# Performance work log

Hardware: AMD Instinct MI355X
Metric: run time of the kernel (lower is better)

The kernel has to match this reference:

```python
import jax, jax.numpy as jnp
import numpy as np

B, ENC, DEC, TSTEPS, PRED = 512, 2048, 1024, 12, 24
IN_DIM = ENC + 1 + TSTEPS  # 2061


def setup_inputs() -> dict:
    key = jax.random.key(0)
    ks = jax.random.split(key, 12)
    s = 0.05  # small init scale for numerical stability
    return {
        "encoder_out": jax.random.normal(ks[0], (B, ENC), jnp.float32),
        "oni_input": jax.random.normal(ks[1], (B, 1), jnp.float32),
        "ssi": jax.random.normal(ks[2], (B, TSTEPS), jnp.float32),
        "W_ih": jax.random.normal(ks[3], (4 * DEC, IN_DIM), jnp.float32) * s,
        "b_ih": jax.random.normal(ks[4], (4 * DEC,), jnp.float32) * s,
        "W_hh": jax.random.normal(ks[5], (4 * DEC, DEC), jnp.float32) * s,
        "b_hh": jax.random.normal(ks[6], (4 * DEC,), jnp.float32) * s,
        "W_l1": jax.random.normal(ks[7], (DEC, DEC * PRED), jnp.float32) * s,
        "b_l1": jax.random.normal(ks[8], (DEC,), jnp.float32) * s,
        "W_l2": jax.random.normal(ks[9], (DEC, DEC), jnp.float32) * s,
        "b_l2": jax.random.normal(ks[10], (DEC,), jnp.float32) * s,
    }


def reference(encoder_out, oni_input, ssi, W_ih, b_ih, W_hh, b_hh, W_l1, b_l1, W_l2, b_l2):
    # cfg.lstm=True, cfg.loss_criterion='enso', dropout p=0 (identity)
    x = jnp.concatenate([encoder_out, oni_input, ssi], axis=1)  # (B, IN_DIM)
    # input is identical every step: precompute input projection once
    x_proj = x @ W_ih.T + b_ih + b_hh  # (B, 4*DEC)
    D = W_hh.shape[1]
    T = W_l1.shape[1] // D
    b = x.shape[0]

    def step(carry, _):
        h, c = carry
        gates = x_proj + h @ W_hh.T  # (B, 4D), PyTorch gate order i,f,g,o
        i, f, g, o = jnp.split(gates, 4, axis=1)
        c = jax.nn.sigmoid(f) * c + jax.nn.sigmoid(i) * jnp.tanh(g)
        h = jax.nn.sigmoid(o) * jnp.tanh(c)
        return (h, c), h

    init = (jnp.zeros((b, D), x.dtype), jnp.zeros((b, D), x.dtype))
    _, hs = jax.lax.scan(step, init, None, length=T)  # (T, B, D)
    # torch.stack(dim=2) then flatten(start_dim=1) -> layout (B, D*T)
    preds = jnp.transpose(hs, (1, 2, 0)).reshape(b, D * T)
    preds = jax.nn.sigmoid(preds @ W_l1.T + b_l1)
    preds = preds @ W_l2.T + b_l2
    return jax.nn.sigmoid(preds)  # 'enso' head; dropout(p=0) is identity
```

## Files before the change

kernel.cpp:

```cpp
#include <hip/hip_runtime.h>
#include <hip/hip_bf16.h>

#define BSZ   512
#define ENCD  2048
#define DECD  1024
#define TST   12
#define PREDT 24
#define INDIM 2061
#define KPAD  2112
#define G4    4096
#define KH    24576

typedef __attribute__((ext_vector_type(8))) short s8v;
typedef __attribute__((ext_vector_type(4))) short s4v;
typedef __attribute__((ext_vector_type(4))) float f4v;

__device__ __forceinline__ short bf16_of(float f) {
  union { float f; unsigned u; } x; x.f = f;
  unsigned r = x.u + 0x7fffu + ((x.u >> 16) & 1u);
  return (short)(r >> 16);
}
__device__ __forceinline__ float sigf(float x) { return 1.f / (1.f + __expf(-x)); }
__device__ __forceinline__ float tanh_(float x) { return 1.f - 2.f / (1.f + __expf(2.f * x)); }

__device__ __forceinline__ int lds_off(int row, int colb) {
  return row * 128 + (colb ^ ((row & 7) << 4));
}


__global__ void prep_x(const float* __restrict__ enc, const float* __restrict__ oni,
                       const float* __restrict__ ssi, short* __restrict__ x_bf) {
  int idx = blockIdx.x * 256 + threadIdx.x;
  if (idx >= BSZ * KPAD) return;
  int b = idx / KPAD, k = idx % KPAD;
  float v = 0.f;
  if (k < ENCD) v = enc[b * ENCD + k];
  else if (k == ENCD) v = oni[b];
  else if (k < INDIM) v = ssi[b * TST + (k - ENCD - 1)];
  x_bf[idx] = bf16_of(v);
}

__global__ void prep_wih(const float* __restrict__ W, short* __restrict__ o) {
  int idx = blockIdx.x * 256 + threadIdx.x;
  int rp = idx / KPAD; int k = idx - rp * KPAD;
  int dblk = rp >> 6, rem = rp & 63, g = rem >> 4, dl = rem & 15;
  int srow = g * 1024 + dblk * 16 + dl;
  float v = (k < INDIM) ? W[(size_t)srow * INDIM + k] : 0.f;
  o[idx] = bf16_of(v);
}

__global__ void prep_whh(const float* __restrict__ W, short* __restrict__ o) {
  int idx = blockIdx.x * 256 + threadIdx.x;
  int rp = idx >> 10; int k = idx & 1023;
  int dblk = rp >> 6, rem = rp & 63, g = rem >> 4, dl = rem & 15;
  int srow = g * 1024 + dblk * 16 + dl;
  o[idx] = bf16_of(W[(size_t)srow * 1024 + k]);
}

__global__ __launch_bounds__(256, 1) void xproj_k(
    const short* __restrict__ x_bf, const short* __restrict__ wih_bf,
    const float* __restrict__ b_ih, const float* __restrict__ b_hh,
    float* __restrict__ xp_p) {
  __shared__ __align__(16) char sA[2][16384];
  __shared__ __align__(16) char sB[2][8192];
  int tid = threadIdx.x, lane = tid & 63, w = tid >> 6;
  int L = blockIdx.x;
  int bm = L >> 6, pb = (L & 7) * 8 + ((L >> 3) & 7);
  const int l4 = lane & 15, lg = lane >> 4;

  s8v aR[4], bR[2];
  auto LOAD = [&](int kt) {
    int kk = kt * 64;
#pragma unroll
    for (int i = 0; i < 4; ++i) {
      int c = tid + i * 256, r = c >> 3, sl = c & 7;
      aR[i] = *(const s8v*)(x_bf + (size_t)(bm * 128 + r) * KPAD + kk + sl * 8);
    }
#pragma unroll
    for (int i = 0; i < 2; ++i) {
      int c = tid + i * 256, r = c >> 3, sl = c & 7;
      bR[i] = *(const s8v*)(wih_bf + (size_t)(pb * 64 + r) * KPAD + kk + sl * 8);
    }
  };
  auto WRITE = [&](int buf) {
#pragma unroll
    for (int i = 0; i < 4; ++i) {
      int c = tid + i * 256, r = c >> 3, sl = c & 7;
      *(s8v*)(sA[buf] + lds_off(r, sl * 16)) = aR[i];
    }
#pragma unroll
    for (int i = 0; i < 2; ++i) {
      int c = tid + i * 256, r = c >> 3, sl = c & 7;
      *(s8v*)(sB[buf] + lds_off(r, sl * 16)) = bR[i];
    }
  };

  f4v acc[2][4] = {};
  LOAD(0); WRITE(0); LOAD(1);
  __syncthreads();
  for (int kt = 0; kt < 33; ++kt) {
    int cur = kt & 1;
    if (kt < 32) WRITE(cur ^ 1);
    if (kt < 31) LOAD(kt + 2);
#pragma unroll
    for (int ks = 0; ks < 2; ++ks) {
      int colb = ks * 64 + lg * 16;
      s8v af[2], bf[4];
#pragma unroll
      for (int mi = 0; mi < 2; ++mi)
        af[mi] = *(const s8v*)(sA[cur] + lds_off(w * 32 + mi * 16 + l4, colb));
#pragma unroll
      for (int ni = 0; ni < 4; ++ni)
        bf[ni] = *(const s8v*)(sB[cur] + lds_off(ni * 16 + l4, colb));
#pragma unroll
      for (int mi = 0; mi < 2; ++mi)
#pragma unroll
        for (int ni = 0; ni < 4; ++ni)
          acc[mi][ni] = __builtin_amdgcn_mfma_f32_16x16x32_bf16(af[mi], bf[ni], acc[mi][ni], 0, 0, 0);
    }
    __syncthreads();
  }
#pragma unroll
  for (int ni = 0; ni < 4; ++ni) {
    int src = ni * 1024 + pb * 16 + l4;
    float bv = b_ih[src] + b_hh[src];
#pragma unroll
    for (int mi = 0; mi < 2; ++mi)
#pragma unroll
      for (int j = 0; j < 4; ++j) {
        int row = bm * 128 + w * 32 + mi * 16 + lg * 4 + j;
        xp_p[(size_t)row * G4 + pb * 64 + ni * 16 + l4] = acc[mi][ni][j] + bv;
      }
  }
}

template <bool FIRST>
__global__ __launch_bounds__(256, 2) void step_k(
    const short* __restrict__ h_in, const short* __restrict__ whh_bf,
    const float* __restrict__ xp_p, float* __restrict__ c_st,
    short* __restrict__ h_out, short* __restrict__ hs_t, int tstep) {
  __shared__ __align__(16) char sB[2][8192];
  __shared__ __align__(16) char sA[4][2][2048];
  int tid = threadIdx.x, lane = tid & 63, w = tid >> 6;
  int L = blockIdx.x;
  int bm = L >> 6, dblk = (L & 7) * 8 + ((L >> 3) & 7);
  const int l4 = lane & 15, lg = lane >> 4;

  f4v acc[4] = {};

  if (!FIRST) {
    const short* hbase = h_in + (size_t)(bm * 64 + w * 16) * DECD;
    const short* bbase = whh_bf + (size_t)(dblk * 64) * DECD;
    s8v aR[2], bR[2];
    auto LOAD = [&](int kt) {
      int kk = kt * 64;
#pragma unroll
      for (int i = 0; i < 2; ++i) {
        int c = lane + i * 64, r = c >> 3, sl = c & 7;
        aR[i] = *(const s8v*)(hbase + (size_t)r * DECD + kk + sl * 8);
      }
#pragma unroll
      for (int i = 0; i < 2; ++i) {
        int c = tid + i * 256, r = c >> 3, sl = c & 7;
        bR[i] = *(const s8v*)(bbase + (size_t)r * DECD + kk + sl * 8);
      }
    };
    auto WRITE = [&](int buf) {
#pragma unroll
      for (int i = 0; i < 2; ++i) {
        int c = lane + i * 64, r = c >> 3, sl = c & 7;
        *(s8v*)(sA[w][buf] + lds_off(r, sl * 16)) = aR[i];
      }
#pragma unroll
      for (int i = 0; i < 2; ++i) {
        int c = tid + i * 256, r = c >> 3, sl = c & 7;
        *(s8v*)(sB[buf] + lds_off(r, sl * 16)) = bR[i];
      }
    };
    LOAD(0); WRITE(0); LOAD(1);
    __syncthreads();
    for (int kt = 0; kt < 16; ++kt) {
      int cur = kt & 1;
      if (kt < 15) WRITE(cur ^ 1);
      if (kt < 14) LOAD(kt + 2);
#pragma unroll
      for (int ks = 0; ks < 2; ++ks) {
        int colb = ks * 64 + lg * 16;
        s8v af = *(const s8v*)(sA[w][cur] + lds_off(l4, colb));
        s8v bf[4];
#pragma unroll
        for (int ni = 0; ni < 4; ++ni)
          bf[ni] = *(const s8v*)(sB[cur] + lds_off(ni * 16 + l4, colb));
#pragma unroll
        for (int ni = 0; ni < 4; ++ni)
          acc[ni] = __builtin_amdgcn_mfma_f32_16x16x32_bf16(af, bf[ni], acc[ni], 0, 0, 0);
      }
      __syncthreads();
    }
  }

  int d = dblk * 16 + l4;
#pragma unroll
  for (int j = 0; j < 4; ++j) {
    int row = bm * 64 + w * 16 + lg * 4 + j;
    size_t xb = (size_t)row * G4 + dblk * 64 + l4;
    float gi = acc[0][j] + xp_p[xb];
    float gf = acc[1][j] + xp_p[xb + 16];
    float gg = acc[2][j] + xp_p[xb + 32];
    float go = acc[3][j] + xp_p[xb + 48];
    size_t cd = (size_t)row * DECD + d;
    float c_old = FIRST ? 0.f : c_st[cd];
    float cn = sigf(gf) * c_old + sigf(gi) * tanh_(gg);
    c_st[cd] = cn;
    float h = sigf(go) * tanh_(cn);
    short hb = bf16_of(h);
    if (tstep < 23) h_out[cd] = hb;
    hs_t[(size_t)tstep * (BSZ * DECD) + cd] = hb;
  }
}

__global__ void transpose_k(const short* __restrict__ hs_t, short* __restrict__ hs) {
  int g = blockIdx.x * 256 + threadIdx.x;
  int row = g >> 10, d = g & 1023;
#pragma unroll
  for (int i = 0; i < 3; ++i) {
    s8v v;
#pragma unroll
    for (int u = 0; u < 8; ++u)
      v[u] = hs_t[(size_t)(i * 8 + u) * (BSZ * DECD) + (size_t)row * DECD + d];
    *(s8v*)(hs + (size_t)row * KH + d * PREDT + i * 8) = v;
  }
}

template <int EPI>
__global__ __launch_bounds__(256, 2) void gemm2_k(
    const short* __restrict__ A, int lda, const float* __restrict__ Bw, int ldb,
    int ntiles, int kchunk, const float* __restrict__ bias1,
    float* __restrict__ Cf, int ldc) {
  __shared__ __align__(16) char sA[2][16384];
  __shared__ __align__(16) char sB[2][16384];
  int tid = threadIdx.x, lane = tid & 63, wid = tid >> 6;
  int wr = wid >> 1, wc = wid & 1, l4 = lane & 15, lg = lane >> 4;
  int bm = blockIdx.x * 128, bn = blockIdx.y * 128;
  int k0 = blockIdx.z * kchunk;
  size_t zoff = (size_t)blockIdx.z * BSZ * (size_t)ldc;
  s8v aR[4]; f4v bR[4][2];
  auto LOAD = [&](int kt) {
    int kk = k0 + kt * 64;
#pragma unroll
    for (int i = 0; i < 4; ++i) {
      int c = tid + i * 256, r = c >> 3, sl = c & 7;
      aR[i] = *(const s8v*)(A + (size_t)(bm + r) * lda + kk + sl * 8);
      const float* src = Bw + (size_t)(bn + r) * ldb + kk + sl * 8;
      bR[i][0] = *(const f4v*)src;
      bR[i][1] = *(const f4v*)(src + 4);
    }
  };
  auto WRITE = [&](int buf) {
#pragma unroll
    for (int i = 0; i < 4; ++i) {
      int c = tid + i * 256, r = c >> 3, sl = c & 7;
      *(s8v*)(sA[buf] + lds_off(r, sl * 16)) = aR[i];
      s8v v;
#pragma unroll
      for (int j = 0; j < 4; ++j) { v[j] = bf16_of(bR[i][0][j]); v[4 + j] = bf16_of(bR[i][1][j]); }
      *(s8v*)(sB[buf] + lds_off(r, sl * 16)) = v;
    }
  };
  f4v acc[4][4] = {};
  LOAD(0); WRITE(0);
  if (ntiles > 1) LOAD(1);
  __syncthreads();
  for (int kt = 0; kt < ntiles; ++kt) {
    int cur = kt & 1;
    if (kt + 1 < ntiles) WRITE(cur ^ 1);
    if (kt + 2 < ntiles) LOAD(kt + 2);
#pragma unroll
    for (int ks = 0; ks < 2; ++ks) {
      int colb = ks * 64 + lg * 16;
      s8v af[4], bf[4];
#pragma unroll
      for (int mi = 0; mi < 4; ++mi)
        af[mi] = *(const s8v*)(sA[cur] + lds_off(wr * 64 + mi * 16 + l4, colb));
#pragma unroll
      for (int ni = 0; ni < 4; ++ni)
        bf[ni] = *(const s8v*)(sB[cur] + lds_off(wc * 64 + ni * 16 + l4, colb));
#pragma unroll
      for (int mi = 0; mi < 4; ++mi)
#pragma unroll
        for (int ni = 0; ni < 4; ++ni)
          acc[mi][ni] = __builtin_amdgcn_mfma_f32_16x16x32_bf16(af[mi], bf[ni], acc[mi][ni], 0, 0, 0);
    }
    __syncthreads();
  }
#pragma unroll
  for (int mi = 0; mi < 4; ++mi)
#pragma unroll
    for (int ni = 0; ni < 4; ++ni)
#pragma unroll
      for (int j = 0; j < 4; ++j) {
        int row = bm + wr * 64 + mi * 16 + lg * 4 + j;
        int col = bn + wc * 64 + ni * 16 + l4;
        float v = acc[mi][ni][j];
        if (EPI == 1) Cf[zoff + (size_t)row * ldc + col] = v;
        else Cf[(size_t)row * ldc + col] = sigf(v + bias1[col]);
      }
}

__global__ void reduce16(const float* __restrict__ part, const float* __restrict__ b_l1,
                         short* __restrict__ z1) {
  int i4 = blockIdx.x * 256 + threadIdx.x;
  int base = i4 * 4;
  int n = base & (DECD - 1);
  f4v s = *(const f4v*)(b_l1 + n);
#pragma unroll
  for (int z = 0; z < 16; ++z) {
    f4v p = *(const f4v*)(part + (size_t)z * (BSZ * DECD) + base);
#pragma unroll
    for (int j = 0; j < 4; ++j) s[j] += p[j];
  }
  s4v o;
#pragma unroll
  for (int j = 0; j < 4; ++j) o[j] = bf16_of(sigf(s[j]));
  *(s4v*)(z1 + base) = o;
}


extern "C" void kernel_launch(void* const* d_in, const int* in_sizes, int n_in,
                              void* d_out, int out_size, void* d_ws, size_t ws_size,
                              hipStream_t stream) {
  const float* enc  = (const float*)d_in[0];
  const float* oni  = (const float*)d_in[1];
  const float* ssi  = (const float*)d_in[2];
  const float* W_ih = (const float*)d_in[3];
  const float* b_ih = (const float*)d_in[4];
  const float* W_hh = (const float*)d_in[5];
  const float* b_hh = (const float*)d_in[6];
  const float* W_l1 = (const float*)d_in[7];
  const float* b_l1 = (const float*)d_in[8];
  const float* W_l2 = (const float*)d_in[9];
  const float* b_l2 = (const float*)d_in[10];
  float* out = (float*)d_out;
  (void)in_sizes; (void)n_in; (void)out_size; (void)ws_size;

  char* ws = (char*)d_ws;
  size_t off = 0;
  auto carve = [&](size_t bytes) { char* p = ws + off; off += (bytes + 255) & ~(size_t)255; return p; };
  short* x_bf   = (short*)carve((size_t)BSZ * KPAD * 2);
  short* wih_bf = (short*)carve((size_t)G4 * KPAD * 2);
  short* whh_bf = (short*)carve((size_t)G4 * DECD * 2);
  float* xp_p   = (float*)carve((size_t)BSZ * G4 * 4);
  short* h0     = (short*)carve((size_t)BSZ * DECD * 2);
  short* h1     = (short*)carve((size_t)BSZ * DECD * 2);
  float* c_st   = (float*)carve((size_t)BSZ * DECD * 4);
  float* part   = (float*)ws;
  if (off < (size_t)16 * BSZ * DECD * 4) off = (((size_t)16 * BSZ * DECD * 4) + 255) & ~(size_t)255;
  short* hs_t   = (short*)carve((size_t)PREDT * BSZ * DECD * 2);
  short* hs     = (short*)carve((size_t)BSZ * KH * 2);
  short* z1     = (short*)carve((size_t)BSZ * DECD * 2);

  prep_x  <<<(BSZ * KPAD) / 256, 256, 0, stream>>>(enc, oni, ssi, x_bf);
  prep_wih<<<(G4 * KPAD) / 256, 256, 0, stream>>>(W_ih, wih_bf);
  prep_whh<<<(G4 * DECD) / 256, 256, 0, stream>>>(W_hh, whh_bf);

  xproj_k<<<256, 256, 0, stream>>>(x_bf, wih_bf, b_ih, b_hh, xp_p);

  step_k<true><<<512, 256, 0, stream>>>(nullptr, whh_bf, xp_p, c_st, h0, hs_t, 0);
  for (int t = 1; t < PREDT; ++t) {
    short* hr = (t & 1) ? h0 : h1;
    short* hw = (t & 1) ? h1 : h0;
    step_k<false><<<512, 256, 0, stream>>>(hr, whh_bf, xp_p, c_st, hw, hs_t, t);
  }

  transpose_k<<<(BSZ * DECD) / 256, 256, 0, stream>>>(hs_t, hs);

  gemm2_k<1><<<dim3(4, 8, 16), 256, 0, stream>>>(hs, KH, W_l1, KH, 24, KH / 16, nullptr, part, DECD);
  reduce16<<<(BSZ * DECD) / 1024, 256, 0, stream>>>(part, b_l1, z1);

  gemm2_k<2><<<dim3(4, 8, 1), 256, 0, stream>>>(z1, DECD, W_l2, DECD, 16, DECD, b_l2, out, DECD);
}
```

Measured before the change: 412.0 us.

## Restructure LSTM step kernel with split-K warps and direct A loads; reorder GEMM grid

The recurrent step kernel now gives each block a 64-row batch tile and a 64-gate column tile. Its four waves split K in two halves, and each wave computes a 32x64 tile, so every W_hh tile staged in LDS feeds twice as many MFMAs. The h operand is read directly from global memory instead of being staged through LDS. Partial sums are reduced through shared memory, and the gate epilogue is remapped so lanes read swizzled LDS rows, which coalesces xp/c/h accesses. The output GEMMs swap grid x/y so blocks sharing a weight tile launch adjacently, aiming for better L2 reuse; unstaged global A loads may add latency.

```diff
diff --git a/kernel.cpp b/kernel.cpp
--- a/kernel.cpp
+++ b/kernel.cpp
@@ -139,75 +139,107 @@
     const short* __restrict__ h_in, const short* __restrict__ whh_bf,
     const float* __restrict__ xp_p, float* __restrict__ c_st,
     short* __restrict__ h_out, short* __restrict__ hs_t, int tstep) {
-  __shared__ __align__(16) char sB[2][8192];
-  __shared__ __align__(16) char sA[4][2][2048];
+  __shared__ __align__(16) char sB[32768];
+  __shared__ __align__(16) char sX[16384];
   int tid = threadIdx.x, lane = tid & 63, w = tid >> 6;
-  int L = blockIdx.x;
-  int bm = L >> 6, dblk = (L & 7) * 8 + ((L >> 3) & 7);
+  int kg = w >> 1, ow = w & 1;
+  int bm = blockIdx.x, cp = blockIdx.y;
   const int l4 = lane & 15, lg = lane >> 4;
 
-  f4v acc[4] = {};
+  f4v acc[2][4] = {};
 
   if (!FIRST) {
-    const short* hbase = h_in + (size_t)(bm * 64 + w * 16) * DECD;
-    const short* bbase = whh_bf + (size_t)(dblk * 64) * DECD;
-    s8v aR[2], bR[2];
-    auto LOAD = [&](int kt) {
-      int kk = kt * 64;
-#pragma unroll
-      for (int i = 0; i < 2; ++i) {
-        int c = lane + i * 64, r = c >> 3, sl = c & 7;
-        aR[i] = *(const s8v*)(hbase + (size_t)r * DECD + kk + sl * 8);
-      }
-#pragma unroll
-      for (int i = 0; i < 2; ++i) {
-        int c = tid + i * 256, r = c >> 3, sl = c & 7;
-        bR[i] = *(const s8v*)(bbase + (size_t)r * DECD + kk + sl * 8);
+    const short* bbase = whh_bf + (size_t)cp * 64 * DECD + kg * 512;
+    const short* abase = h_in + (size_t)(bm * 64 + ow * 32) * DECD + kg * 512;
+    char* myB = sB + kg * 16384;
+    int lc = tid & 127;
+    s8v st[4];
+    auto LOADB = [&](int kt) {
+#pragma unroll
+      for (int i = 0; i < 4; ++i) {
+        int c = lc + i * 128, r = c >> 3, sl = c & 7;
+        st[i] = *(const s8v*)(bbase + (size_t)r * DECD + kt * 64 + sl * 8);
       }
     };
-    auto WRITE = [&](int buf) {
-#pragma unroll
-      for (int i = 0; i < 2; ++i) {
-        int c = lane + i * 64, r = c >> 3, sl = c & 7;
-        *(s8v*)(sA[w][buf] + lds_off(r, sl * 16)) = aR[i];
-      }
-#pragma unroll
-      for (int i = 0; i < 2; ++i) {
-        int c = tid + i * 256, r = c >> 3, sl = c & 7;
-        *(s8v*)(sB[buf] + lds_off(r, sl * 16)) = bR[i];
+    auto WRITEB = [&](int buf) {
+      char* p = myB + buf * 8192;
+#pragma unroll
+      for (int i = 0; i < 4; ++i) {
+        int c = lc + i * 128, r = c >> 3, sl = c & 7;
+        *(s8v*)(p + lds_off(r, sl * 16)) = st[i];
       }
     };
-    LOAD(0); WRITE(0); LOAD(1);
+    LOADB(0); WRITEB(0); LOADB(1);
     __syncthreads();
-    for (int kt = 0; kt < 16; ++kt) {
+    for (int kt = 0; kt < 8; ++kt) {
       int cur = kt & 1;
-      if (kt < 15) WRITE(cur ^ 1);
-      if (kt < 14) LOAD(kt + 2);
+      if (kt < 7) WRITEB(cur ^ 1);
+      if (kt < 6) LOADB(kt + 2);
+      char* p = myB + cur * 8192;
 #pragma unroll
       for (int ks = 0; ks < 2; ++ks) {
-        int colb = ks * 64 + lg * 16;
-        s8v af = *(const s8v*)(sA[w][cur] + lds_off(l4, colb));
-        s8v bf[4];
+        s8v af[2], bf[4];
+#pragma unroll
+        for (int mi = 0; mi < 2; ++mi)
+          af[mi] = *(const s8v*)(abase + (size_t)(mi * 16 + l4) * DECD + kt * 64 + ks * 32 + lg * 8);
 #pragma unroll
         for (int ni = 0; ni < 4; ++ni)
-          bf[ni] = *(const s8v*)(sB[cur] + lds_off(ni * 16 + l4, colb));
-#pragma unroll
-        for (int ni = 0; ni < 4; ++ni)
-          acc[ni] = __builtin_amdgcn_mfma_f32_16x16x32_bf16(af, bf[ni], acc[ni], 0, 0, 0);
+          bf[ni] = *(const s8v*)(p + lds_off(ni * 16 + l4, ks * 64 + lg * 16));
+#pragma unroll
+        for (int mi = 0; mi < 2; ++mi)
+#pragma unroll
+          for (int ni = 0; ni < 4; ++ni)
+            acc[mi][ni] = __builtin_amdgcn_mfma_f32_16x16x32_bf16(af[mi], bf[ni], acc[mi][ni], 0, 0, 0);
       }
       __syncthreads();
     }
-  }
-
-  int d = dblk * 16 + l4;
-#pragma unroll
-  for (int j = 0; j < 4; ++j) {
-    int row = bm * 64 + w * 16 + lg * 4 + j;
-    size_t xb = (size_t)row * G4 + dblk * 64 + l4;
-    float gi = acc[0][j] + xp_p[xb];
-    float gf = acc[1][j] + xp_p[xb + 16];
-    float gg = acc[2][j] + xp_p[xb + 32];
-    float go = acc[3][j] + xp_p[xb + 48];
+    if (kg == 1) {
+#pragma unroll
+      for (int mi = 0; mi < 2; ++mi)
+#pragma unroll
+        for (int ni = 0; ni < 4; ++ni)
+#pragma unroll
+          for (int j = 0; j < 4; ++j)
+            *(float*)(sX + ow * 8192 + ((mi * 4 + ni) * 4 + j) * 256 + lane * 4) = acc[mi][ni][j];
+    }
+    __syncthreads();
+    if (kg == 0) {
+#pragma unroll
+      for (int mi = 0; mi < 2; ++mi)
+#pragma unroll
+        for (int ni = 0; ni < 4; ++ni) {
+#pragma unroll
+          for (int j = 0; j < 4; ++j) {
+            float v = acc[mi][ni][j] +
+                      *(const float*)(sX + ow * 8192 + ((mi * 4 + ni) * 4 + j) * 256 + lane * 4);
+            int row = ow * 32 + mi * 16 + lg * 4 + j;
+            int col = ni * 16 + l4;
+            *(float*)(sB + row * 256 + ((col ^ ((row & 3) << 4)) * 4)) = v;
+          }
+        }
+    }
+    __syncthreads();
+  }
+
+#pragma unroll
+  for (int q = 0; q < 4; ++q) {
+    int idx = tid + q * 256;
+    int r = idx >> 4, dl = idx & 15;
+    int row = bm * 64 + r;
+    size_t xb = (size_t)row * G4 + cp * 64 + dl;
+    float g0 = 0.f, g1 = 0.f, g2 = 0.f, g3 = 0.f;
+    if (!FIRST) {
+      int sw = (r & 3) << 4;
+      g0 = *(const float*)(sB + r * 256 + (((0  + dl) ^ sw) * 4));
+      g1 = *(const float*)(sB + r * 256 + (((16 + dl) ^ sw) * 4));
+      g2 = *(const float*)(sB + r * 256 + (((32 + dl) ^ sw) * 4));
+      g3 = *(const float*)(sB + r * 256 + (((48 + dl) ^ sw) * 4));
+    }
+    float gi = g0 + xp_p[xb];
+    float gf = g1 + xp_p[xb + 16];
+    float gg = g2 + xp_p[xb + 32];
+    float go = g3 + xp_p[xb + 48];
+    int d = cp * 16 + dl;
     size_t cd = (size_t)row * DECD + d;
     float c_old = FIRST ? 0.f : c_st[cd];
     float cn = sigf(gf) * c_old + sigf(gi) * tanh_(gg);
@@ -241,7 +273,7 @@
   __shared__ __align__(16) char sB[2][16384];
   int tid = threadIdx.x, lane = tid & 63, wid = tid >> 6;
   int wr = wid >> 1, wc = wid & 1, l4 = lane & 15, lg = lane >> 4;
-  int bm = blockIdx.x * 128, bn = blockIdx.y * 128;
+  int bn = blockIdx.x * 128, bm = blockIdx.y * 128;
   int k0 = blockIdx.z * kchunk;
   size_t zoff = (size_t)blockIdx.z * BSZ * (size_t)ldc;
   s8v aR[4]; f4v bR[4][2];
@@ -365,17 +397,17 @@
 
   xproj_k<<<256, 256, 0, stream>>>(x_bf, wih_bf, b_ih, b_hh, xp_p);
 
-  step_k<true><<<512, 256, 0, stream>>>(nullptr, whh_bf, xp_p, c_st, h0, hs_t, 0);
+  step_k<true><<<dim3(8, 64), 256, 0, stream>>>(nullptr, whh_bf, xp_p, c_st, h0, hs_t, 0);
   for (int t = 1; t < PREDT; ++t) {
     short* hr = (t & 1) ? h0 : h1;
     short* hw = (t & 1) ? h1 : h0;
-    step_k<false><<<512, 256, 0, stream>>>(hr, whh_bf, xp_p, c_st, hw, hs_t, t);
+    step_k<false><<<dim3(8, 64), 256, 0, stream>>>(hr, whh_bf, xp_p, c_st, hw, hs_t, t);
   }
 
   transpose_k<<<(BSZ * DECD) / 256, 256, 0, stream>>>(hs_t, hs);
 
-  gemm2_k<1><<<dim3(4, 8, 16), 256, 0, stream>>>(hs, KH, W_l1, KH, 24, KH / 16, nullptr, part, DECD);
+  gemm2_k<1><<<dim3(8, 4, 16), 256, 0, stream>>>(hs, KH, W_l1, KH, 24, KH / 16, nullptr, part, DECD);
   reduce16<<<(BSZ * DECD) / 1024, 256, 0, stream>>>(part, b_l1, z1);
 
-  gemm2_k<2><<<dim3(4, 8, 1), 256, 0, stream>>>(z1, DECD, W_l2, DECD, 16, DECD, b_l2, out, DECD);
-}
+  gemm2_k<2><<<dim3(8, 4, 1), 256, 0, stream>>>(z1, DECD, W_l2, DECD, 16, DECD, b_l2, out, DECD);
+}
```

After: 541.7 us. +31.5%, slower.

## Deepen LSTM step K-tile, prefetch gate inputs early, remap grids for weight locality

Applied to the files above, without the earlier changes.

The recurrent step kernel now loads 128-wide K tiles with a 16-row XOR swizzle, which halves the number of pipeline iterations and barriers. It also prefetches the x-projection gate values and the previous cell state into registers before the MFMA loop, so their global latency overlaps the matmul. The step grid becomes 2D (column-block by batch-block), replacing the old interleaved block mapping. In the output GEMMs the grid axes are swapped so that blocks sharing a weight tile are adjacent. LDS usage per block doubles, which may reduce occupancy, and the extra prefetch registers add pressure.

```diff
diff --git a/kernel.cpp b/kernel.cpp
--- a/kernel.cpp
+++ b/kernel.cpp
@@ -25,6 +25,9 @@
 
 __device__ __forceinline__ int lds_off(int row, int colb) {
   return row * 128 + (colb ^ ((row & 7) << 4));
+}
+__device__ __forceinline__ int lds2(int row, int colb) {
+  return row * 256 + (colb ^ ((row & 15) << 4));
 }
 
 
@@ -139,58 +142,70 @@
     const short* __restrict__ h_in, const short* __restrict__ whh_bf,
     const float* __restrict__ xp_p, float* __restrict__ c_st,
     short* __restrict__ h_out, short* __restrict__ hs_t, int tstep) {
-  __shared__ __align__(16) char sB[2][8192];
-  __shared__ __align__(16) char sA[4][2][2048];
+  __shared__ __align__(16) char sB[2][16384];
+  __shared__ __align__(16) char sA[4][2][4096];
   int tid = threadIdx.x, lane = tid & 63, w = tid >> 6;
-  int L = blockIdx.x;
-  int bm = L >> 6, dblk = (L & 7) * 8 + ((L >> 3) & 7);
+  int cp = blockIdx.x, bm = blockIdx.y;
   const int l4 = lane & 15, lg = lane >> 4;
+  const int d = cp * 16 + l4;
+
+  float xg[4][4], cpre[4];
+#pragma unroll
+  for (int j = 0; j < 4; ++j) {
+    int row = bm * 64 + w * 16 + lg * 4 + j;
+    size_t xb = (size_t)row * G4 + cp * 64 + l4;
+    xg[j][0] = xp_p[xb];
+    xg[j][1] = xp_p[xb + 16];
+    xg[j][2] = xp_p[xb + 32];
+    xg[j][3] = xp_p[xb + 48];
+    cpre[j] = FIRST ? 0.f : c_st[(size_t)row * DECD + d];
+  }
 
   f4v acc[4] = {};
 
   if (!FIRST) {
-    const short* hbase = h_in + (size_t)(bm * 64 + w * 16) * DECD;
-    const short* bbase = whh_bf + (size_t)(dblk * 64) * DECD;
-    s8v aR[2], bR[2];
+    const short* bbase = whh_bf + (size_t)cp * 64 * DECD;
+    const short* abase = h_in + (size_t)(bm * 64 + w * 16) * DECD;
+    s8v aR[4], bR[4];
     auto LOAD = [&](int kt) {
-      int kk = kt * 64;
-#pragma unroll
-      for (int i = 0; i < 2; ++i) {
-        int c = lane + i * 64, r = c >> 3, sl = c & 7;
-        aR[i] = *(const s8v*)(hbase + (size_t)r * DECD + kk + sl * 8);
-      }
-#pragma unroll
-      for (int i = 0; i < 2; ++i) {
-        int c = tid + i * 256, r = c >> 3, sl = c & 7;
+      int kk = kt * 128;
+#pragma unroll
+      for (int i = 0; i < 4; ++i) {
+        int c = lane + i * 64, r = c >> 4, sl = c & 15;
+        aR[i] = *(const s8v*)(abase + (size_t)r * DECD + kk + sl * 8);
+      }
+#pragma unroll
+      for (int i = 0; i < 4; ++i) {
+        int c = tid + i * 256, r = c >> 4, sl = c & 15;
         bR[i] = *(const s8v*)(bbase + (size_t)r * DECD + kk + sl * 8);
       }
     };
     auto WRITE = [&](int buf) {
 #pragma unroll
-      for (int i = 0; i < 2; ++i) {
-        int c = lane + i * 64, r = c >> 3, sl = c & 7;
-        *(s8v*)(sA[w][buf] + lds_off(r, sl * 16)) = aR[i];
-      }
-#pragma unroll
-      for (int i = 0; i < 2; ++i) {
-        int c = tid + i * 256, r = c >> 3, sl = c & 7;
-        *(s8v*)(sB[buf] + lds_off(r, sl * 16)) = bR[i];
+      for (int i = 0; i < 4; ++i) {
+        int c = lane + i * 64, r = c >> 4, sl = c & 15;
+        *(s8v*)(sA[w][buf] + lds2(r, sl * 16)) = aR[i];
+      }
+#pragma unroll
+      for (int i = 0; i < 4; ++i) {
+        int c = tid + i * 256, r = c >> 4, sl = c & 15;
+        *(s8v*)(sB[buf] + lds2(r, sl * 16)) = bR[i];
       }
     };
     LOAD(0); WRITE(0); LOAD(1);
     __syncthreads();
-    for (int kt = 0; kt < 16; ++kt) {
+    for (int kt = 0; kt < 8; ++kt) {
       int cur = kt & 1;
-      if (kt < 15) WRITE(cur ^ 1);
-      if (kt < 14) LOAD(kt + 2);
-#pragma unroll
-      for (int ks = 0; ks < 2; ++ks) {
+      if (kt < 7) WRITE(cur ^ 1);
+      if (kt < 6) LOAD(kt + 2);
+#pragma unroll
+      for (int ks = 0; ks < 4; ++ks) {
         int colb = ks * 64 + lg * 16;
-        s8v af = *(const s8v*)(sA[w][cur] + lds_off(l4, colb));
+        s8v af = *(const s8v*)(sA[w][cur] + lds2(l4, colb));
         s8v bf[4];
 #pragma unroll
         for (int ni = 0; ni < 4; ++ni)
-          bf[ni] = *(const s8v*)(sB[cur] + lds_off(ni * 16 + l4, colb));
+          bf[ni] = *(const s8v*)(sB[cur] + lds2(ni * 16 + l4, colb));
 #pragma unroll
         for (int ni = 0; ni < 4; ++ni)
           acc[ni] = __builtin_amdgcn_mfma_f32_16x16x32_bf16(af, bf[ni], acc[ni], 0, 0, 0);
@@ -199,20 +214,17 @@
     }
   }
 
-  int d = dblk * 16 + l4;
 #pragma unroll
   for (int j = 0; j < 4; ++j) {
     int row = bm * 64 + w * 16 + lg * 4 + j;
-    size_t xb = (size_t)row * G4 + dblk * 64 + l4;
-    float gi = acc[0][j] + xp_p[xb];
-    float gf = acc[1][j] + xp_p[xb + 16];
-    float gg = acc[2][j] + xp_p[xb + 32];
-    float go = acc[3][j] + xp_p[xb + 48];
+    float gi = xg[j][0] + acc[0][j];
+    float gf = xg[j][1] + acc[1][j];
+    float gg = xg[j][2] + acc[2][j];
+    float go = xg[j][3] + acc[3][j];
+    float cn = sigf(gf) * cpre[j] + sigf(gi) * tanh_(gg);
+    float h = sigf(go) * tanh_(cn);
     size_t cd = (size_t)row * DECD + d;
-    float c_old = FIRST ? 0.f : c_st[cd];
-    float cn = sigf(gf) * c_old + sigf(gi) * tanh_(gg);
     c_st[cd] = cn;
-    float h = sigf(go) * tanh_(cn);
     short hb = bf16_of(h);
     if (tstep < 23) h_out[cd] = hb;
     hs_t[(size_t)tstep * (BSZ * DECD) + cd] = hb;
@@ -241,7 +253,7 @@
   __shared__ __align__(16) char sB[2][16384];
   int tid = threadIdx.x, lane = tid & 63, wid = tid >> 6;
   int wr = wid >> 1, wc = wid & 1, l4 = lane & 15, lg = lane >> 4;
-  int bm = blockIdx.x * 128, bn = blockIdx.y * 128;
+  int bn = blockIdx.x * 128, bm = blockIdx.y * 128;
   int k0 = blockIdx.z * kchunk;
   size_t zoff = (size_t)blockIdx.z * BSZ * (size_t)ldc;
   s8v aR[4]; f4v bR[4][2];
@@ -365,17 +377,17 @@
 
   xproj_k<<<256, 256, 0, stream>>>(x_bf, wih_bf, b_ih, b_hh, xp_p);
 
-  step_k<true><<<512, 256, 0, stream>>>(nullptr, whh_bf, xp_p, c_st, h0, hs_t, 0);
+  step_k<true><<<dim3(64, 8), 256, 0, stream>>>(nullptr, whh_bf, xp_p, c_st, h0, hs_t, 0);
   for (int t = 1; t < PREDT; ++t) {
     short* hr = (t & 1) ? h0 : h1;
     short* hw = (t & 1) ? h1 : h0;
-    step_k<false><<<512, 256, 0, stream>>>(hr, whh_bf, xp_p, c_st, hw, hs_t, t);
+    step_k<false><<<dim3(64, 8), 256, 0, stream>>>(hr, whh_bf, xp_p, c_st, hw, hs_t, t);
   }
 
   transpose_k<<<(BSZ * DECD) / 256, 256, 0, stream>>>(hs_t, hs);
 
-  gemm2_k<1><<<dim3(4, 8, 16), 256, 0, stream>>>(hs, KH, W_l1, KH, 24, KH / 16, nullptr, part, DECD);
+  gemm2_k<1><<<dim3(8, 4, 16), 256, 0, stream>>>(hs, KH, W_l1, KH, 24, KH / 16, nullptr, part, DECD);
   reduce16<<<(BSZ * DECD) / 1024, 256, 0, stream>>>(part, b_l1, z1);
 
-  gemm2_k<2><<<dim3(4, 8, 1), 256, 0, stream>>>(z1, DECD, W_l2, DECD, 16, DECD, b_l2, out, DECD);
-}
+  gemm2_k<2><<<dim3(8, 4, 1), 256, 0, stream>>>(z1, DECD, W_l2, DECD, 16, DECD, b_l2, out, DECD);
+}
```

New measurement: 421.4 us. 2.3% more time.

## Enlarge LSTM step tile to 128 rows and prefetch gate inputs early

Applied to the files above, without the earlier changes.

Each recurrent step block now covers 128 batch rows instead of 64, with every wave computing two 16-row MFMA tiles. This halves the grid to 256 blocks and halves how often each W_hh tile is reloaded across blocks. The x-projection gates and previous cell state are loaded into registers before the K loop so their latency overlaps the GEMM. The gemm2 grid is also reordered so blocks that share an A row-tile run next to each other. In exchange the step kernel uses more registers and LDS, and with fewer blocks the 256 CUs may be less fully occupied.

```diff
diff --git a/kernel.cpp b/kernel.cpp
--- a/kernel.cpp
+++ b/kernel.cpp
@@ -140,24 +140,38 @@
     const float* __restrict__ xp_p, float* __restrict__ c_st,
     short* __restrict__ h_out, short* __restrict__ hs_t, int tstep) {
   __shared__ __align__(16) char sB[2][8192];
-  __shared__ __align__(16) char sA[4][2][2048];
+  __shared__ __align__(16) char sA[4][2][4096];
   int tid = threadIdx.x, lane = tid & 63, w = tid >> 6;
-  int L = blockIdx.x;
-  int bm = L >> 6, dblk = (L & 7) * 8 + ((L >> 3) & 7);
+  int cp = blockIdx.x, bm = blockIdx.y;
   const int l4 = lane & 15, lg = lane >> 4;
-
-  f4v acc[4] = {};
+  const int d = cp * 16 + l4;
+
+  float xg[2][4][4], cpre[2][4];
+#pragma unroll
+  for (int mi = 0; mi < 2; ++mi)
+#pragma unroll
+    for (int j = 0; j < 4; ++j) {
+      int row = bm * 128 + w * 32 + mi * 16 + lg * 4 + j;
+      size_t xb = (size_t)row * G4 + cp * 64 + l4;
+      xg[mi][j][0] = xp_p[xb];
+      xg[mi][j][1] = xp_p[xb + 16];
+      xg[mi][j][2] = xp_p[xb + 32];
+      xg[mi][j][3] = xp_p[xb + 48];
+      cpre[mi][j] = FIRST ? 0.f : c_st[(size_t)row * DECD + d];
+    }
+
+  f4v acc[2][4] = {};
 
   if (!FIRST) {
-    const short* hbase = h_in + (size_t)(bm * 64 + w * 16) * DECD;
-    const short* bbase = whh_bf + (size_t)(dblk * 64) * DECD;
-    s8v aR[2], bR[2];
+    const short* bbase = whh_bf + (size_t)cp * 64 * DECD;
+    const short* abase = h_in + (size_t)(bm * 128 + w * 32) * DECD;
+    s8v aR[4], bR[2];
     auto LOAD = [&](int kt) {
       int kk = kt * 64;
 #pragma unroll
-      for (int i = 0; i < 2; ++i) {
+      for (int i = 0; i < 4; ++i) {
         int c = lane + i * 64, r = c >> 3, sl = c & 7;
-        aR[i] = *(const s8v*)(hbase + (size_t)r * DECD + kk + sl * 8);
+        aR[i] = *(const s8v*)(abase + (size_t)r * DECD + kk + sl * 8);
       }
 #pragma unroll
       for (int i = 0; i < 2; ++i) {
@@ -167,7 +181,7 @@
     };
     auto WRITE = [&](int buf) {
 #pragma unroll
-      for (int i = 0; i < 2; ++i) {
+      for (int i = 0; i < 4; ++i) {
         int c = lane + i * 64, r = c >> 3, sl = c & 7;
         *(s8v*)(sA[w][buf] + lds_off(r, sl * 16)) = aR[i];
       }
@@ -186,37 +200,40 @@
 #pragma unroll
       for (int ks = 0; ks < 2; ++ks) {
         int colb = ks * 64 + lg * 16;
-        s8v af = *(const s8v*)(sA[w][cur] + lds_off(l4, colb));
-        s8v bf[4];
+        s8v af[2], bf[4];
+#pragma unroll
+        for (int mi = 0; mi < 2; ++mi)
+          af[mi] = *(const s8v*)(sA[w][cur] + lds_off(mi * 16 + l4, colb));
 #pragma unroll
         for (int ni = 0; ni < 4; ++ni)
           bf[ni] = *(const s8v*)(sB[cur] + lds_off(ni * 16 + l4, colb));
 #pragma unroll
-        for (int ni = 0; ni < 4; ++ni)
-          acc[ni] = __builtin_amdgcn_mfma_f32_16x16x32_bf16(af, bf[ni], acc[ni], 0, 0, 0);
+        for (int mi = 0; mi < 2; ++mi)
+#pragma unroll
+          for (int ni = 0; ni < 4; ++ni)
+            acc[mi][ni] = __builtin_amdgcn_mfma_f32_16x16x32_bf16(af[mi], bf[ni], acc[mi][ni], 0, 0, 0);
       }
       __syncthreads();
     }
   }
 
-  int d = dblk * 16 + l4;
-#pragma unroll
-  for (int j = 0; j < 4; ++j) {
-    int row = bm * 64 + w * 16 + lg * 4 + j;
-    size_t xb = (size_t)row * G4 + dblk * 64 + l4;
-    float gi = acc[0][j] + xp_p[xb];
-    float gf = acc[1][j] + xp_p[xb + 16];
-    float gg = acc[2][j] + xp_p[xb + 32];
-    float go = acc[3][j] + xp_p[xb + 48];
-    size_t cd = (size_t)row * DECD + d;
-    float c_old = FIRST ? 0.f : c_st[cd];
-    float cn = sigf(gf) * c_old + sigf(gi) * tanh_(gg);
-    c_st[cd] = cn;
-    float h = sigf(go) * tanh_(cn);
-    short hb = bf16_of(h);
-    if (tstep < 23) h_out[cd] = hb;
-    hs_t[(size_t)tstep * (BSZ * DECD) + cd] = hb;
-  }
+#pragma unroll
+  for (int mi = 0; mi < 2; ++mi)
+#pragma unroll
+    for (int j = 0; j < 4; ++j) {
+      int row = bm * 128 + w * 32 + mi * 16 + lg * 4 + j;
+      float gi = xg[mi][j][0] + acc[mi][0][j];
+      float gf = xg[mi][j][1] + acc[mi][1][j];
+      float gg = xg[mi][j][2] + acc[mi][2][j];
+      float go = xg[mi][j][3] + acc[mi][3][j];
+      float cn = sigf(gf) * cpre[mi][j] + sigf(gi) * tanh_(gg);
+      float h = sigf(go) * tanh_(cn);
+      size_t cd = (size_t)row * DECD + d;
+      c_st[cd] = cn;
+      short hb = bf16_of(h);
+      if (tstep < 23) h_out[cd] = hb;
+      hs_t[(size_t)tstep * (BSZ * DECD) + cd] = hb;
+    }
 }
 
 __global__ void transpose_k(const short* __restrict__ hs_t, short* __restrict__ hs) {
@@ -241,7 +258,7 @@
   __shared__ __align__(16) char sB[2][16384];
   int tid = threadIdx.x, lane = tid & 63, wid = tid >> 6;
   int wr = wid >> 1, wc = wid & 1, l4 = lane & 15, lg = lane >> 4;
-  int bm = blockIdx.x * 128, bn = blockIdx.y * 128;
+  int bn = blockIdx.x * 128, bm = blockIdx.y * 128;
   int k0 = blockIdx.z * kchunk;
   size_t zoff = (size_t)blockIdx.z * BSZ * (size_t)ldc;
   s8v aR[4]; f4v bR[4][2];
@@ -365,17 +382,17 @@
 
   xproj_k<<<256, 256, 0, stream>>>(x_bf, wih_bf, b_ih, b_hh, xp_p);
 
-  step_k<true><<<512, 256, 0, stream>>>(nullptr, whh_bf, xp_p, c_st, h0, hs_t, 0);
+  step_k<true><<<dim3(64, 4), 256, 0, stream>>>(nullptr, whh_bf, xp_p, c_st, h0, hs_t, 0);
   for (int t = 1; t < PREDT; ++t) {
     short* hr = (t & 1) ? h0 : h1;
     short* hw = (t & 1) ? h1 : h0;
-    step_k<false><<<512, 256, 0, stream>>>(hr, whh_bf, xp_p, c_st, hw, hs_t, t);
+    step_k<false><<<dim3(64, 4), 256, 0, stream>>>(hr, whh_bf, xp_p, c_st, hw, hs_t, t);
   }
 
   transpose_k<<<(BSZ * DECD) / 256, 256, 0, stream>>>(hs_t, hs);
 
-  gemm2_k<1><<<dim3(4, 8, 16), 256, 0, stream>>>(hs, KH, W_l1, KH, 24, KH / 16, nullptr, part, DECD);
+  gemm2_k<1><<<dim3(8, 4, 16), 256, 0, stream>>>(hs, KH, W_l1, KH, 24, KH / 16, nullptr, part, DECD);
   reduce16<<<(BSZ * DECD) / 1024, 256, 0, stream>>>(part, b_l1, z1);
 
-  gemm2_k<2><<<dim3(4, 8, 1), 256, 0, stream>>>(z1, DECD, W_l2, DECD, 16, DECD, b_l2, out, DECD);
-}
+  gemm2_k<2><<<dim3(8, 4, 1), 256, 0, stream>>>(z1, DECD, W_l2, DECD, 16, DECD, b_l2, out, DECD);
+}
```

New measurement: 412.6 us, median of 2. No clear change (+0.1%).
